# Kernel optimization log

Hardware: AMD Instinct MI355X
Metric: run time of the kernel (lower is better)

Reference implementation:

```python
import jax, jax.numpy as jnp
import numpy as np
import math

B, L, N = 8, 2048, 512
H = 16                                  # router hidden_dim
C = min(16, max(2, int(math.sqrt(N))))  # num_centers = 16
D = 64                                  # d_core
STATIC_TOPK = max(32, int(math.sqrt(N) * 2))  # 45


def setup_inputs() -> dict:
    key = jax.random.key(0)
    ks = jax.random.split(key, 32)
    r = lambda i, shape, s=0.05: jax.random.normal(ks[i], shape, jnp.float32) * s
    return dict(
        x=jax.random.normal(ks[0], (B, L, N), jnp.float32),
        var_embed=r(1, (1, N, H), 0.1),
        temp_w=r(2, (2, H)), temp_b=jnp.zeros((H,), jnp.float32),
        q_w=r(3, (2 * H, H)), q_b=jnp.zeros((H,), jnp.float32),
        k_w=r(4, (2 * H, H)), k_b=jnp.zeros((H,), jnp.float32),
        imp_w=r(5, (2 * H, 1)), imp_b=jnp.zeros((1,), jnp.float32),
        cluster_score=r(6, (N, C), 1.0),
        varproj_w=r(7, (C, D)), varproj_b=jnp.zeros((D,), jnp.float32),
        cp1_w=r(8, (D, D)), cp1_b=jnp.zeros((D,), jnp.float32),
        cp2_w=r(9, (D, D)), cp2_b=jnp.zeros((D,), jnp.float32),
        cg_w=r(10, (N, C * D)), cg_b=jnp.zeros((C * D,), jnp.float32),
        gate_w=r(11, (2 * N, N)), gate_b=jnp.zeros((N,), jnp.float32),
        fus_w=r(12, (N, N)), fus_b=jnp.zeros((N,), jnp.float32),
        ln_g=jnp.ones((N,), jnp.float32), ln_b=jnp.zeros((N,), jnp.float32),
    )


def _build_static_mask(x):
    # torch no_grad block: std over batch dim, unbiased (ddof=1)
    xs = jax.lax.stop_gradient(x)
    x_avg = xs.mean(axis=0)                       # [L, N]
    x_std = jnp.std(xs, axis=0, ddof=1) + 1e-5    # [L, N]
    normed = x_avg / x_std
    sim = normed.T @ normed                       # [N, N]
    sim = sim.at[jnp.diag_indices(N)].set(-1e9)
    _, idx = jax.lax.top_k(sim, STATIC_TOPK)      # [N, STATIC_TOPK]
    return jnp.zeros((N, N), bool).at[jnp.arange(N)[:, None], idx].set(True)


def reference(x, var_embed, temp_w, temp_b, q_w, q_b, k_w, k_b, imp_w, imp_b,
              cluster_score, varproj_w, varproj_b, cp1_w, cp1_b, cp2_w, cp2_b,
              cg_w, cg_b, gate_w, gate_b, fus_w, fus_b, ln_g, ln_b):
    mask = _build_static_mask(x)                  # [N, N] bool

    # ---- SparseVariableRouter ----
    x_var = x.transpose(0, 2, 1)                  # [B, N, L]
    mean = x_var.mean(-1, keepdims=True)
    std = jnp.sqrt(jnp.var(x_var, -1, ddof=1, keepdims=True) + 1e-5)
    time_emb = jnp.concatenate([mean, std], -1) @ temp_w + temp_b   # [B, N, H]
    static_emb = jnp.broadcast_to(var_embed, (x.shape[0], N, H))
    var_fused = jnp.concatenate([static_emb, time_emb], -1)         # [B, N, 2H]
    importance = jax.nn.sigmoid(var_fused @ imp_w + imp_b)[..., 0][:, None, :]  # [B,1,N]
    Q = var_fused @ q_w + q_b
    K = var_fused @ k_w + k_b
    sim = jnp.einsum('bnh,bmh->bnm', Q, K) / math.sqrt(H)
    sim = jnp.where(mask[None], sim, -1e9)
    attn = jax.nn.softmax(sim, axis=-1)
    routed = jnp.einsum('bnm,bml->bnl', attn, x_var).transpose(0, 2, 1)  # [B, L, N]
    ring_out = importance * routed + (1.0 - importance) * x

    # ---- multi-center mixing ----
    summary = x.mean(1)                                        # [B, N]
    center_tokens = (summary @ cg_w + cg_b).reshape(-1, C, D)  # [B, C, D]
    cw = jax.nn.softmax(cluster_score, axis=-1)                # [N, C]
    x_center = jnp.einsum('bln,nc->blc', x, cw) @ varproj_w + varproj_b  # [B, L, D]
    cu = center_tokens[:, None, :, :] + x_center[:, :, None, :]          # [B, L, C, D]
    cu = jax.nn.gelu(cu @ cp1_w + cp1_b, approximate=False) @ cp2_w + cp2_b
    center_to_var = jnp.einsum('blcd,nc->bln', cu, cw)         # [B, L, N]

    # ---- gated fusion + layernorm ----
    gate = jax.nn.sigmoid(jnp.concatenate([ring_out, center_to_var], -1) @ gate_w + gate_b)
    fused = gate * ring_out + (1.0 - gate) * center_to_var
    fused = fused @ fus_w + fus_b
    h = fused + x
    mu = h.mean(-1, keepdims=True)
    var = jnp.var(h, -1, keepdims=True)            # biased, as torch LayerNorm
    out = (h - mu) / jnp.sqrt(var + 1e-5) * ln_g + ln_b
    return out
```

## Files before the change

kernel.cpp:

```cpp
#include <hip/hip_runtime.h>

#define B_ 8
#define L_ 2048
#define N_ 512
#define H_ 16
#define C_ 16
#define D_ 64
#define TK_ 45
#define KS_ 16

typedef __attribute__((ext_vector_type(8))) short bf16x8;
typedef __attribute__((ext_vector_type(4))) float f32x4;

__device__ __forceinline__ float sigmoidf_(float v) { return 1.f / (1.f + expf(-v)); }

__device__ __forceinline__ short f2bf(float f) {
  union { float f; unsigned u; } v; v.f = f;
  unsigned r = (v.u + 0x7fffu + ((v.u >> 16) & 1u)) >> 16;
  return (short)r;
}
__device__ __forceinline__ float bf2f(short s) {
  union { unsigned u; float f; } v; v.u = ((unsigned)(unsigned short)s) << 16;
  return v.f;
}
__device__ __forceinline__ void gload16(const void* g, void* l) {
  __builtin_amdgcn_global_load_lds((const __attribute__((address_space(1))) unsigned int*)g,
                                   (__attribute__((address_space(3))) unsigned int*)l, 16, 0, 0);
}

__global__ __launch_bounds__(512) void k_pre(const float* __restrict__ x,
                                             const float* __restrict__ var_embed,
                                             const float* __restrict__ temp_w,
                                             const float* __restrict__ temp_b,
                                             const float* __restrict__ q_w,
                                             const float* __restrict__ q_b,
                                             const float* __restrict__ k_w,
                                             const float* __restrict__ k_b,
                                             const float* __restrict__ imp_w,
                                             const float* __restrict__ imp_b,
                                             const float* __restrict__ cs,
                                             const float* __restrict__ cp2_w,
                                             const float* __restrict__ cp2_b,
                                             const float* __restrict__ vp_b,
                                             const float* __restrict__ vp_w,
                                             const float* __restrict__ cp1_w,
                                             float* __restrict__ normed,
                                             float* __restrict__ psum,
                                             float* __restrict__ psq,
                                             short* __restrict__ xbf,
                                             float* __restrict__ veq,
                                             float* __restrict__ vek,
                                             float* __restrict__ abc,
                                             float* __restrict__ vei,
                                             float* __restrict__ cw,
                                             float* __restrict__ misc) {
  int blk = blockIdx.x, t = threadIdx.x;
  if (blk < 256) {
    int l0 = blk * 8;
    int n = t;
    float row_s[8] = {}, row_ss[8] = {};
#pragma unroll
    for (int b = 0; b < B_; ++b) {
      float bs = 0.f, bss = 0.f;
#pragma unroll
      for (int r = 0; r < 8; ++r) {
        float v = x[((size_t)b * L_ + l0 + r) * N_ + n];
        bs += v; bss += v * v;
        row_s[r] += v; row_ss[r] += v * v;
        xbf[((size_t)b * L_ + l0 + r) * N_ + n] = f2bf(v);
      }
      psum[((size_t)b * 256 + blk) * N_ + n] = bs;
      psq [((size_t)b * 256 + blk) * N_ + n] = bss;
    }
#pragma unroll
    for (int r = 0; r < 8; ++r) {
      float mean = row_s[r] * (1.f / B_);
      float var  = fmaxf((row_ss[r] - row_s[r] * mean) * (1.f / (B_ - 1)), 0.f);
      normed[(l0 + r) * N_ + n] = mean / (sqrtf(var) + 1e-5f);
    }
    return;
  }
  if (t >= 256) return;
  if (blk < 288) {
    int gid = (blk - 256) * 256 + t;
    int n = gid >> 4, h = gid & 15;
    float aq = 0.f, ak = 0.f;
#pragma unroll
    for (int i = 0; i < 16; ++i) {
      float ve = var_embed[n * 16 + i];
      aq += ve * q_w[i * 16 + h];
      ak += ve * k_w[i * 16 + h];
    }
    veq[gid] = aq;
    vek[gid] = ak;
  } else if (blk == 288) {
    if (t < 16) {
      int h = t;
      float Aq = 0.f, Bq = 0.f, Cq = 0.f, Ak = 0.f, Bk = 0.f, Ck = 0.f;
#pragma unroll
      for (int j = 0; j < 16; ++j) {
        float qw = q_w[(16 + j) * 16 + h];
        float kw = k_w[(16 + j) * 16 + h];
        Aq += temp_w[j] * qw; Bq += temp_w[16 + j] * qw; Cq += temp_b[j] * qw;
        Ak += temp_w[j] * kw; Bk += temp_w[16 + j] * kw; Ck += temp_b[j] * kw;
      }
      abc[h]      = Aq; abc[16 + h] = Bq; abc[32 + h] = Cq + q_b[h];
      abc[48 + h] = Ak; abc[64 + h] = Bk; abc[80 + h] = Ck + k_b[h];
    } else if (t == 16) {
      float aI = 0.f, bI = 0.f, cI = 0.f;
#pragma unroll
      for (int j = 0; j < 16; ++j) {
        float iw = imp_w[16 + j];
        aI += temp_w[j] * iw; bI += temp_w[16 + j] * iw; cI += temp_b[j] * iw;
      }
      abc[96] = aI; abc[97] = bI; abc[98] = cI + imp_b[0];
    }
  } else if (blk < 291) {
    int n = (blk - 289) * 256 + t;
    float a = 0.f;
#pragma unroll
    for (int i = 0; i < 16; ++i)
      a += var_embed[n * 16 + i] * imp_w[i];
    vei[n] = a;
  } else {
#pragma unroll
    for (int u = 0; u < 2; ++u) {
      int n = t + u * 256;
      float v[16], mx = -3e38f;
#pragma unroll
      for (int c = 0; c < 16; ++c) { v[c] = cs[n * 16 + c]; mx = fmaxf(mx, v[c]); }
      float s = 0.f;
#pragma unroll
      for (int c = 0; c < 16; ++c) { v[c] = expf(v[c] - mx); s += v[c]; }
      float inv = 1.f / s;
#pragma unroll
      for (int c = 0; c < 16; ++c) cw[n * 16 + c] = v[c] * inv;
    }
    if (t < 64) {
      float a = 0.f;
#pragma unroll 8
      for (int d = 0; d < 64; ++d) a += cp2_w[t * 64 + d];
      misc[t] = a;
      float vb = 0.f;
#pragma unroll 8
      for (int e = 0; e < 64; ++e) vb += vp_b[e] * cp1_w[e * 64 + t];
      misc[80 + t] = vb;
    }
    if (t == 0) {
      float bsum = 0.f;
      for (int d = 0; d < 64; ++d) bsum += cp2_b[d];
      misc[64] = bsum;
    }
#pragma unroll
    for (int u = 0; u < 4; ++u) {
      int i = t + u * 256;
      int c = i >> 6, d = i & 63;
      float a = 0.f;
#pragma unroll 8
      for (int e = 0; e < 64; ++e) a += vp_w[c * 64 + e] * cp1_w[e * 64 + d];
      misc[96 + i] = a;
    }
  }
}

__global__ __launch_bounds__(256) void k_sim(const float* __restrict__ nrm,
                                             float* __restrict__ simP) {
  __shared__ float As[32 * 64];
  __shared__ float Bs[32 * 64];
  int bx = blockIdx.x;
  int ks = bx >> 6, tile = bx & 63;
  int bi = tile & 7, bj = tile >> 3;
  int t = threadIdx.x, tx = t & 15, ty = t >> 4;
  float acc[4][4] = {};
  int k0 = ks * (L_ / KS_);
  for (int kt = 0; kt < (L_ / KS_) / 32; ++kt) {
    for (int e = t; e < 2048; e += 256) {
      int kk = e >> 6, i = e & 63;
      int krow = k0 + kt * 32 + kk;
      As[e] = nrm[krow * N_ + bi * 64 + i];
      Bs[e] = nrm[krow * N_ + bj * 64 + i];
    }
    __syncthreads();
#pragma unroll
    for (int kk = 0; kk < 32; ++kk) {
      float4 a = *(const float4*)(As + kk * 64 + ty * 4);
      float4 b = *(const float4*)(Bs + kk * 64 + tx * 4);
      float av[4] = {a.x, a.y, a.z, a.w};
      float bv[4] = {b.x, b.y, b.z, b.w};
#pragma unroll
      for (int i = 0; i < 4; ++i)
#pragma unroll
        for (int j = 0; j < 4; ++j)
          acc[i][j] += av[i] * bv[j];
    }
    __syncthreads();
  }
  float* outp = simP + (size_t)ks * (N_ * N_);
#pragma unroll
  for (int i = 0; i < 4; ++i) {
    int row = bi * 64 + ty * 4 + i;
    float4 o = {acc[i][0], acc[i][1], acc[i][2], acc[i][3]};
    *(float4*)(outp + row * N_ + bj * 64 + tx * 4) = o;
  }
}

__global__ __launch_bounds__(256) void k_simred(const float* __restrict__ simP,
                                                float* __restrict__ sim,
                                                const float* __restrict__ psum,
                                                const float* __restrict__ psq,
                                                float* __restrict__ psumR,
                                                float* __restrict__ psqR) {
  int t = threadIdx.x;
  if (blockIdx.x < 256) {
    int gid = blockIdx.x * 256 + t;
    float4 s = {0.f, 0.f, 0.f, 0.f};
#pragma unroll
    for (int ksi = 0; ksi < KS_; ++ksi) {
      float4 p = *(const float4*)(simP + (size_t)ksi * (N_ * N_) + gid * 4);
      s.x += p.x; s.y += p.y; s.z += p.z; s.w += p.w;
    }
    *(float4*)(sim + gid * 4) = s;
    return;
  }
  int tid = (blockIdx.x - 256) * 256 + t;
  const float* src = (tid < 4096) ? psum : psq;
  float* dst = (tid < 4096) ? psumR : psqR;
  int id = tid & 4095;
  int b = id >> 9, n = id & 511;
  float a = 0.f;
#pragma unroll 8
  for (int c = 0; c < 256; ++c)
    a += src[((size_t)b * 256 + c) * N_ + n];
  dst[id] = a;
}

__global__ __launch_bounds__(256) void k_tf(
    const float* __restrict__ sim, int* __restrict__ idx_t,
    const float* __restrict__ psumR, const float* __restrict__ psqR,
    const float* __restrict__ veq, const float* __restrict__ vek,
    const float* __restrict__ abc, const float* __restrict__ vei,
    float* __restrict__ Q, float* __restrict__ Kv,
    float* __restrict__ imp, float* __restrict__ summary) {
  int t = threadIdx.x;
  if (blockIdx.x < 128) {
    int lane = t & 63, wv = t >> 6;
    int n = blockIdx.x * 4 + wv;
    unsigned sv[8];
#pragma unroll
    for (int u = 0; u < 8; ++u) {
      int idx = u * 64 + lane;
      float f = (idx == n) ? -3e38f : sim[n * N_ + idx];
      unsigned xb = __float_as_uint(f);
      sv[u] = (xb & 0x80000000u) ? ~xb : (xb | 0x80000000u);
    }
    unsigned thr = 0u;
#pragma unroll
    for (int b = 31; b >= 0; --b) {
      unsigned cand = thr | (1u << b);
      int cnt = 0;
#pragma unroll
      for (int u = 0; u < 8; ++u)
        cnt += __popcll(__ballot(sv[u] >= cand));
      if (cnt >= TK_) thr = cand;
    }
    int cgt = 0;
#pragma unroll
    for (int u = 0; u < 8; ++u)
      cgt += __popcll(__ballot(sv[u] > thr));
    int need = TK_ - cgt;
    unsigned long long lt_mask = (lane == 0) ? 0ull : (~0ull >> (64 - lane));
    int written = 0, tie_seen = 0;
#pragma unroll
    for (int u = 0; u < 8; ++u) {
      bool gt = sv[u] > thr;
      bool eq = sv[u] == thr;
      unsigned long long me = __ballot(eq);
      bool sel = gt || (eq && (tie_seen + __popcll(me & lt_mask)) < need);
      unsigned long long ms = __ballot(sel);
      int pos = written + __popcll(ms & lt_mask);
      if (sel) idx_t[pos * N_ + n] = u * 64 + lane;
      written += __popcll(ms);
      tie_seen += __popcll(me);
    }
    return;
  }
  int gid = (blockIdx.x - 128) * 256 + t;
  int b = gid >> 9, n = gid & 511;
  float s  = psumR[gid];
  float ss = psqR[gid];
  float mean = s * (1.f / L_);
  float var  = fmaxf((ss - s * mean) * (1.f / (L_ - 1)), 0.f);
  float stdv = sqrtf(var + 1e-5f);
  summary[b * N_ + n] = mean;
#pragma unroll
  for (int h = 0; h < 16; ++h) {
    Q[(b * N_ + n) * 16 + h]  = veq[n * 16 + h] + mean * abc[h]      + stdv * abc[16 + h] + abc[32 + h];
    Kv[(b * N_ + n) * 16 + h] = vek[n * 16 + h] + mean * abc[48 + h] + stdv * abc[64 + h] + abc[80 + h];
  }
  imp[b * N_ + n] = sigmoidf_(vei[n] + mean * abc[96] + stdv * abc[97] + abc[98]);
}

__global__ __launch_bounds__(256) void k_wprep(const float* __restrict__ gate_w,
                                               const float* __restrict__ fus_w,
                                               const float* __restrict__ cw,
                                               const float* __restrict__ misc,
                                               const float* __restrict__ summ,
                                               const float* __restrict__ cg_w,
                                               const float* __restrict__ cg_b,
                                               short* __restrict__ wt_gate,
                                               short* __restrict__ wt_fus,
                                               short* __restrict__ w2t,
                                               short* __restrict__ cwb,
                                               float* __restrict__ ctP) {
  __shared__ float tile[32][33];
  __shared__ float ssum[8][64];
  int blk = blockIdx.x, t = threadIdx.x;
  if (blk < 512) {
    const float* W = (blk < 256) ? gate_w : fus_w;
    short* Wt = (blk < 256) ? wt_gate : wt_fus;
    int ldd = (blk < 256) ? 1024 : 512;
    int b2 = blk & 255;
    int bk = b2 >> 4, bn = b2 & 15;
    int c = t & 31, r = t >> 5;
    for (int rr = r; rr < 32; rr += 8)
      tile[rr][c] = W[(size_t)(bk * 32 + rr) * 512 + bn * 32 + c];
    __syncthreads();
    for (int rr = r; rr < 32; rr += 8)
      Wt[(size_t)(bn * 32 + rr) * ldd + bk * 32 + c] = f2bf(tile[c][rr]);
  } else if (blk < 544) {
    int gid = (blk - 512) * 256 + t;
    int c = gid >> 9, n = gid & 511;
    float a = 0.f;
    for (int m = 0; m < 512; ++m)
      a += cw[m * 16 + c] * gate_w[(size_t)(512 + m) * 512 + n];
    wt_gate[(size_t)n * 1024 + 512 + c] = f2bf(a);
    wt_gate[(size_t)n * 1024 + 528 + c] = 0;
  } else if (blk < 672) {
    int gid = (blk - 544) * 256 + t;
    int d = gid >> 9, m = gid & 511;
    float a = 0.f;
#pragma unroll
    for (int c = 0; c < 16; ++c)
      a += cw[m * 16 + c] * misc[96 + c * 64 + d];
    w2t[d * 512 + m] = f2bf(a);
  } else if (blk < 736) {
    int gid = (blk - 672) * 256 + t;
    int n = gid >> 5, kk = gid & 31;
    cwb[gid] = (kk < 16) ? f2bf(cw[n * 16 + kk]) : (short)0;
  } else {
    int bx = blk - 736;
    int oc = bx & 31;
    int nc = bx >> 5;
    int n0 = nc * 64;
    for (int e = t; e < 512; e += 256)
      ssum[e >> 6][e & 63] = summ[(e >> 6) * 512 + n0 + (e & 63)];
    __syncthreads();
    int b = t >> 5, ol = t & 31;
    int o = oc * 32 + ol;
    float acc = (nc == 0) ? cg_b[o] : 0.f;
#pragma unroll 8
    for (int k = 0; k < 64; ++k)
      acc += ssum[b][k] * cg_w[(size_t)(n0 + k) * 1024 + o];
    ctP[(nc * 8 + b) * 1024 + o] = acc;
  }
}

__global__ __launch_bounds__(256) void k_caxc(const float* __restrict__ ctP,
                                              const float* __restrict__ cp1_w,
                                              const float* __restrict__ cp1_b,
                                              const float* __restrict__ misc,
                                              float* __restrict__ ctp,
                                              const float* __restrict__ Q,
                                              const float* __restrict__ Kv,
                                              const int* __restrict__ idx_t,
                                              short* __restrict__ At,
                                              const short* __restrict__ xbf,
                                              const short* __restrict__ w2t,
                                              float* __restrict__ xcp) {
  __shared__ float cts[256];
  __shared__ short rowbuf[4][512];
  __shared__ __align__(16) short As[2][64 * 32];
  __shared__ __align__(16) short Bs[2][64 * 32];
  int blk = blockIdx.x, t = threadIdx.x;
  if (blk < 32) {
    int row0 = blk * 4;
    int b = row0 >> 4, c0 = row0 & 15;
    {
      int idx = (c0 + (t >> 6)) * 64 + (t & 63);
      float a = 0.f;
#pragma unroll
      for (int p = 0; p < 8; ++p) a += ctP[(p * 8 + b) * 1024 + idx];
      cts[t] = a;
    }
    __syncthreads();
    int lr = t >> 6, d2 = t & 63;
    float a = cp1_b[d2] + misc[80 + d2];
#pragma unroll 8
    for (int d = 0; d < 64; ++d) a += cts[lr * 64 + d] * cp1_w[d * 64 + d2];
    ctp[(row0 + lr) * 64 + d2] = a;
  } else if (blk < 32 + 1024) {
    int w = t >> 6, j = t & 63;
    int bn = (blk - 32) * 4 + w;
    int b = bn >> 9, n = bn & (N_ - 1);
    ((int4*)rowbuf[w])[j] = int4{0, 0, 0, 0};
    float s = -3e38f;
    int m = 0;
    if (j < TK_) {
      m = idx_t[j * N_ + n];
      const float* qp = Q + (b * N_ + n) * H_;
      const float* kp = Kv + (b * N_ + m) * H_;
      float a = 0.f;
#pragma unroll
      for (int h = 0; h < H_; ++h) a += qp[h] * kp[h];
      s = a * 0.25f;
    }
    float mx = s;
#pragma unroll
    for (int o = 32; o > 0; o >>= 1) mx = fmaxf(mx, __shfl_xor(mx, o));
    float e = (j < TK_) ? expf(s - mx) : 0.f;
    float sum = e;
#pragma unroll
    for (int o = 32; o > 0; o >>= 1) sum += __shfl_xor(sum, o);
    __syncthreads();
    if (j < TK_) rowbuf[w][m] = f2bf(e / sum);
    __syncthreads();
    ((int4*)(At + (size_t)bn * 512))[j] = ((int4*)rowbuf[w])[j];
  } else {
    int lane = t & 63, w = t >> 6;
    int lo = lane & 15, hi = lane >> 4;
    int row0 = (blk - 1056) * 64;
    f32x4 acc[4] = {};
    int rA = t >> 2, cA = (t & 3) ^ ((rA >> 1) & 3);
    const short* srcA = xbf + (size_t)(row0 + rA) * 512 + cA * 8;
    const short* srcB = w2t + (size_t)rA * 512 + cA * 8;
    int gl = (lo >> 1) & 3;
    int foff = (lo * 4 + (hi ^ gl)) * 8;
    gload16(srcA, As[0] + t * 8);
    gload16(srcB, Bs[0] + t * 8);
    __syncthreads();
    int cur = 0;
    for (int kt = 0; kt < 16; ++kt) {
      if (kt < 15) {
        gload16(srcA + (kt + 1) * 32, As[cur ^ 1] + t * 8);
        gload16(srcB + (kt + 1) * 32, Bs[cur ^ 1] + t * 8);
      }
      bf16x8 b = *(const bf16x8*)(Bs[cur] + (w * 64) * 8 + foff);
#pragma unroll
      for (int m = 0; m < 4; ++m) {
        bf16x8 a = *(const bf16x8*)(As[cur] + (m * 64) * 8 + foff);
        acc[m] = __builtin_amdgcn_mfma_f32_16x16x32_bf16(a, b, acc[m], 0, 0, 0);
      }
      __syncthreads();
      cur ^= 1;
    }
#pragma unroll
    for (int m = 0; m < 4; ++m)
#pragma unroll
      for (int j = 0; j < 4; ++j) {
        int row = row0 + m * 16 + hi * 4 + j;
        int col = w * 16 + lo;
        xcp[(size_t)row * 64 + col] = acc[m][j];
      }
  }
}

__global__ __launch_bounds__(512) void k_sg(const short* __restrict__ xbf,
                                            const short* __restrict__ At,
                                            const float* __restrict__ imp,
                                            short* __restrict__ abuf,
                                            const float* __restrict__ xcp,
                                            const float* __restrict__ ctp,
                                            const float* __restrict__ misc) {
  __shared__ __align__(16) short As[2][128 * 32];
  __shared__ __align__(16) short Bs[2][128 * 32];
  int blk = blockIdx.x, t = threadIdx.x;
  int lane = t & 63, w = t >> 6;
  if (blk < 512) {
    int lo = lane & 15, hi = lane >> 4;
    int b = blk >> 6;
    int tile = blk & 63;
    int bm = tile >> 2, bn = tile & 3;
    int row0 = b * L_ + bm * 128, n0 = bn * 128;
    int wm = w >> 2, wn = w & 3;
    f32x4 acc[4][2] = {};
    int rs = t >> 2, cs = (t & 3) ^ ((rs >> 1) & 3);
    const short* sA = xbf + (size_t)(row0 + rs) * 512 + cs * 8;
    const short* sB = At + ((size_t)b * N_ + n0 + rs) * 512 + cs * 8;
    int gl = (lo >> 1) & 3;
    int foff = (lo * 4 + (hi ^ gl)) * 8;
    gload16(sA, As[0] + t * 8);
    gload16(sB, Bs[0] + t * 8);
    __syncthreads();
    int cur = 0;
    for (int i = 0; i < 16; ++i) {
      if (i < 15) {
        gload16(sA + (i + 1) * 32, As[cur ^ 1] + t * 8);
        gload16(sB + (i + 1) * 32, Bs[cur ^ 1] + t * 8);
      }
      bf16x8 a[4], bb[2];
#pragma unroll
      for (int m = 0; m < 4; ++m)
        a[m] = *(const bf16x8*)(As[cur] + (wm * 64 + m * 16) * 32 + foff);
#pragma unroll
      for (int n = 0; n < 2; ++n)
        bb[n] = *(const bf16x8*)(Bs[cur] + (wn * 32 + n * 16) * 32 + foff);
#pragma unroll
      for (int m = 0; m < 4; ++m)
#pragma unroll
        for (int n = 0; n < 2; ++n)
          acc[m][n] = __builtin_amdgcn_mfma_f32_16x16x32_bf16(a[m], bb[n], acc[m][n], 0, 0, 0);
      __syncthreads();
      cur ^= 1;
    }
#pragma unroll
    for (int m = 0; m < 4; ++m) {
      int rbase = row0 + wm * 64 + m * 16 + hi * 4;
#pragma unroll
      for (int j = 0; j < 4; ++j) {
        int row = rbase + j;
#pragma unroll
        for (int n = 0; n < 2; ++n) {
          int col = n0 + wn * 32 + n * 16 + lo;
          float iv = imp[b * N_ + col];
          float xv = bf2f(xbf[(size_t)row * 512 + col]);
          abuf[(size_t)row * 1024 + col] = f2bf(iv * acc[m][n][j] + (1.f - iv) * xv);
        }
      }
    }
  } else {
    int row = (blk - 512) * 8 + w;
    int b = row >> 11;
    float v = xcp[(size_t)row * 64 + lane];
    float wgt = misc[lane];
    float bias = misc[64];
    float sval = 0.f;
#pragma unroll
    for (int c = 0; c < 16; ++c) {
      float u = ctp[(b * 16 + c) * 64 + lane] + v;
      float g = 0.5f * u * (1.f + erff(u * 0.70710678118654752f));
      float a = g * wgt;
#pragma unroll
      for (int o = 32; o > 0; o >>= 1) a += __shfl_xor(a, o);
      if (lane == c) sval = a + bias;
    }
    if (lane < 32)
      abuf[(size_t)row * 1024 + 512 + lane] = (lane < 16) ? f2bf(sval) : (short)0;
  }
}

__global__ __launch_bounds__(512) void k_gemm_gate(const short* __restrict__ abuf,
                                                   const short* __restrict__ wt,
                                                   const short* __restrict__ cwb,
                                                   const float* __restrict__ gate_b,
                                                   short* __restrict__ fused_bf) {
  __shared__ __align__(16) short As[2][128 * 32];
  __shared__ __align__(16) short Bs[2][128 * 32];
  int t = threadIdx.x, lane = t & 63, w = t >> 6;
  int lo = lane & 15, hi = lane >> 4;
  int bm = blockIdx.x >> 2, bn = blockIdx.x & 3;
  int row0 = bm * 128, n0 = bn * 128;
  int wm = w >> 2, wn = w & 3;
  f32x4 acc[4][2] = {};
  f32x4 acc2[4][2] = {};
  int rs = t >> 2, cs = (t & 3) ^ ((rs >> 1) & 3);
  const short* sA = abuf + (size_t)(row0 + rs) * 1024 + cs * 8;
  const short* sB = wt + (size_t)(n0 + rs) * 1024 + cs * 8;
  int gl = (lo >> 1) & 3;
  int foff = (lo * 4 + (hi ^ gl)) * 8;
  gload16(sA + 16 * 32, As[0] + t * 8);
  gload16(cwb + (size_t)(n0 + rs) * 32 + cs * 8, Bs[0] + t * 8);
  gload16(sA, As[1] + t * 8);
  gload16(sB, Bs[1] + t * 8);
  __syncthreads();
  {
    bf16x8 a[4], bb[2];
#pragma unroll
    for (int m = 0; m < 4; ++m)
      a[m] = *(const bf16x8*)(As[0] + (wm * 64 + m * 16) * 32 + foff);
#pragma unroll
    for (int n = 0; n < 2; ++n)
      bb[n] = *(const bf16x8*)(Bs[0] + (wn * 32 + n * 16) * 32 + foff);
#pragma unroll
    for (int m = 0; m < 4; ++m)
#pragma unroll
      for (int n = 0; n < 2; ++n)
        acc2[m][n] = __builtin_amdgcn_mfma_f32_16x16x32_bf16(a[m], bb[n], acc2[m][n], 0, 0, 0);
  }
  __syncthreads();
  int cur = 1;
  for (int i = 1; i <= 17; ++i) {
    if (i < 17) {
      gload16(sA + i * 32, As[cur ^ 1] + t * 8);
      gload16(sB + i * 32, Bs[cur ^ 1] + t * 8);
    }
    bf16x8 a[4], bb[2];
#pragma unroll
    for (int m = 0; m < 4; ++m)
      a[m] = *(const bf16x8*)(As[cur] + (wm * 64 + m * 16) * 32 + foff);
#pragma unroll
    for (int n = 0; n < 2; ++n)
      bb[n] = *(const bf16x8*)(Bs[cur] + (wn * 32 + n * 16) * 32 + foff);
#pragma unroll
    for (int m = 0; m < 4; ++m)
#pragma unroll
      for (int n = 0; n < 2; ++n)
        acc[m][n] = __builtin_amdgcn_mfma_f32_16x16x32_bf16(a[m], bb[n], acc[m][n], 0, 0, 0);
    __syncthreads();
    cur ^= 1;
  }
#pragma unroll
  for (int m = 0; m < 4; ++m) {
    int rbase = row0 + wm * 64 + m * 16 + hi * 4;
#pragma unroll
    for (int j = 0; j < 4; ++j) {
      int row = rbase + j;
#pragma unroll
      for (int n = 0; n < 2; ++n) {
        int col = n0 + wn * 32 + n * 16 + lo;
        float g = sigmoidf_(acc[m][n][j] + gate_b[col]);
        float ringv = bf2f(abuf[(size_t)row * 1024 + col]);
        fused_bf[(size_t)row * 512 + col] = f2bf(g * ringv + (1.f - g) * acc2[m][n][j]);
      }
    }
  }
}

__global__ __launch_bounds__(512) void k_gemm_fus(const short* __restrict__ fused_bf,
                                                  const short* __restrict__ wtf,
                                                  const float* __restrict__ x,
                                                  const float* __restrict__ fus_b,
                                                  const float* __restrict__ ln_g,
                                                  const float* __restrict__ ln_b,
                                                  float* __restrict__ out) {
  __shared__ __align__(16) short As[2][64 * 32];
  __shared__ __align__(16) short Bs[2][512 * 32];
  __shared__ float Ssh[8][64], Qsh[8][64];
  __shared__ float mus[64], rss[64];
  int t = threadIdx.x, lane = t & 63, w = t >> 6;
  int lo = lane & 15, hi = lane >> 4;
  int row0 = blockIdx.x * 64;
  f32x4 acc[4][4] = {};
  int pA = w * 64 + lane;
  int rA = pA >> 2, cA = (pA & 3) ^ ((rA >> 1) & 3);
  const short* srcA = fused_bf + (size_t)(row0 + rA) * 512 + cA * 8;
  int rB[4], cB[4];
  const short* srcB[4];
#pragma unroll
  for (int q = 0; q < 4; ++q) {
    int pB = w * 256 + q * 64 + lane;
    rB[q] = pB >> 2; cB[q] = (pB & 3) ^ ((rB[q] >> 1) & 3);
    srcB[q] = wtf + (size_t)rB[q] * 512 + cB[q] * 8;
  }
  int gl = (lo >> 1) & 3;
  int foff = (lo * 4 + (hi ^ gl)) * 8;
  if (w < 4) gload16(srcA, As[0] + pA * 8);
#pragma unroll
  for (int q = 0; q < 4; ++q)
    gload16(srcB[q], Bs[0] + (w * 256 + q * 64) * 8);
  __syncthreads();
  int cur = 0;
  for (int i = 0; i < 16; ++i) {
    if (i < 15) {
      int kt = i + 1;
      if (w < 4) gload16(srcA + kt * 32, As[cur ^ 1] + pA * 8);
#pragma unroll
      for (int q = 0; q < 4; ++q)
        gload16(srcB[q] + kt * 32, Bs[cur ^ 1] + (w * 256 + q * 64) * 8);
    }
    bf16x8 a[4], b[4];
#pragma unroll
    for (int m = 0; m < 4; ++m)
      a[m] = *(const bf16x8*)(As[cur] + (m * 64) * 8 + foff);
#pragma unroll
    for (int n = 0; n < 4; ++n)
      b[n] = *(const bf16x8*)(Bs[cur] + (w * 256 + n * 64) * 8 + foff);
#pragma unroll
    for (int m = 0; m < 4; ++m)
#pragma unroll
      for (int n = 0; n < 4; ++n)
        acc[m][n] = __builtin_amdgcn_mfma_f32_16x16x32_bf16(a[m], b[n], acc[m][n], 0, 0, 0);
    __syncthreads();
    cur ^= 1;
  }
#pragma unroll
  for (int m = 0; m < 4; ++m) {
#pragma unroll
    for (int j = 0; j < 4; ++j) {
      int rl = m * 16 + hi * 4 + j;
      int row = row0 + rl;
      float ps = 0.f, pq = 0.f;
#pragma unroll
      for (int n = 0; n < 4; ++n) {
        int col = w * 64 + n * 16 + lo;
        float h = acc[m][n][j] + fus_b[col] + x[(size_t)row * 512 + col];
        acc[m][n][j] = h;
        ps += h; pq += h * h;
      }
#pragma unroll
      for (int o = 1; o < 16; o <<= 1) {
        ps += __shfl_xor(ps, o);
        pq += __shfl_xor(pq, o);
      }
      if (lo == 0) { Ssh[w][rl] = ps; Qsh[w][rl] = pq; }
    }
  }
  __syncthreads();
  if (t < 64) {
    float s = 0.f, q = 0.f;
#pragma unroll
    for (int ww = 0; ww < 8; ++ww) { s += Ssh[ww][t]; q += Qsh[ww][t]; }
    float mu = s * (1.f / N_);
    float var = q * (1.f / N_) - mu * mu;
    mus[t] = mu;
    rss[t] = rsqrtf(fmaxf(var, 0.f) + 1e-5f);
  }
  __syncthreads();
#pragma unroll
  for (int m = 0; m < 4; ++m) {
#pragma unroll
    for (int j = 0; j < 4; ++j) {
      int rl = m * 16 + hi * 4 + j;
      int row = row0 + rl;
      float mu = mus[rl], rs = rss[rl];
#pragma unroll
      for (int n = 0; n < 4; ++n) {
        int col = w * 64 + n * 16 + lo;
        out[(size_t)row * 512 + col] = (acc[m][n][j] - mu) * rs * ln_g[col] + ln_b[col];
      }
    }
  }
}

extern "C" void kernel_launch(void* const* d_in, const int* in_sizes, int n_in,
                              void* d_out, int out_size, void* d_ws, size_t ws_size,
                              hipStream_t stream) {
  (void)in_sizes; (void)n_in; (void)out_size; (void)ws_size;
  const float* x         = (const float*)d_in[0];
  const float* var_embed = (const float*)d_in[1];
  const float* temp_w    = (const float*)d_in[2];
  const float* temp_b    = (const float*)d_in[3];
  const float* q_w       = (const float*)d_in[4];
  const float* q_b       = (const float*)d_in[5];
  const float* k_w       = (const float*)d_in[6];
  const float* k_b       = (const float*)d_in[7];
  const float* imp_w     = (const float*)d_in[8];
  const float* imp_b     = (const float*)d_in[9];
  const float* cluster   = (const float*)d_in[10];
  const float* vp_w      = (const float*)d_in[11];
  const float* vp_b      = (const float*)d_in[12];
  const float* cp1_w     = (const float*)d_in[13];
  const float* cp1_b     = (const float*)d_in[14];
  const float* cp2_w     = (const float*)d_in[15];
  const float* cp2_b     = (const float*)d_in[16];
  const float* cg_w      = (const float*)d_in[17];
  const float* cg_b      = (const float*)d_in[18];
  const float* gate_w    = (const float*)d_in[19];
  const float* gate_b    = (const float*)d_in[20];
  const float* fus_w     = (const float*)d_in[21];
  const float* fus_b     = (const float*)d_in[22];
  const float* ln_g      = (const float*)d_in[23];
  const float* ln_b      = (const float*)d_in[24];
  float* out = (float*)d_out;
  float* ws  = (float*)d_ws;

  float* normed = ws + 0;
  int*   idx_t  = (int*)(ws + 1310720);
  float* Qb     = ws + 1335296;
  float* Kb     = ws + 1400832;
  float* impb   = ws + 1466368;
  float* summ   = ws + 1470464;
  float* cw     = ws + 1658880;
  float* ctp    = ws + 1675264;
  float* misc   = ws + 1683456;
  short* w2t    = (short*)(ws + 1693696);
  short* cwb    = (short*)(ws + 1710080);
  short* abuf     = (short*)(ws + 1720320);
  short* fused_bf = (short*)(ws + 10108928);
  short* wt_gate  = (short*)(ws + 14303232);
  short* wt_fus   = (short*)(ws + 14565376);
  float* ctP      = ws + 15220736;
  short* At       = (short*)(ws + 15286272);
  float* sim      = ws + 16334848;
  float* veq      = ws + 16596992;
  float* vek      = ws + 16605184;
  float* abc      = ws + 16613376;
  float* vei      = ws + 16613504;
  float* psum     = ws + 17000000;
  float* psq      = ws + 18100000;
  float* psumR    = ws + 19200000;
  float* psqR     = ws + 19210000;
  float* simP = (float*)abuf;
  float* xcp  = normed;
  short* xbf  = fused_bf;

  k_pre<<<292, 512, 0, stream>>>(x, var_embed, temp_w, temp_b, q_w, q_b, k_w, k_b,
                                 imp_w, imp_b, cluster, cp2_w, cp2_b, vp_b, vp_w,
                                 cp1_w, normed, psum, psq, xbf, veq, vek, abc, vei,
                                 cw, misc);
  k_sim<<<64 * KS_, 256, 0, stream>>>(normed, simP);
  k_simred<<<288, 256, 0, stream>>>(simP, sim, psum, psq, psumR, psqR);
  k_tf<<<144, 256, 0, stream>>>(sim, idx_t, psumR, psqR, veq, vek, abc, vei,
                                Qb, Kb, impb, summ);
  k_wprep<<<992, 256, 0, stream>>>(gate_w, fus_w, cw, misc, summ, cg_w, cg_b,
                                   wt_gate, wt_fus, w2t, cwb, ctP);
  k_caxc<<<1312, 256, 0, stream>>>(ctP, cp1_w, cp1_b, misc, ctp, Qb, Kb, idx_t,
                                   At, xbf, w2t, xcp);
  k_sg<<<2560, 512, 0, stream>>>(xbf, At, impb, abuf, xcp, ctp, misc);
  k_gemm_gate<<<512, 512, 0, stream>>>(abuf, wt_gate, cwb, gate_b, fused_bf);
  k_gemm_fus<<<256, 512, 0, stream>>>(fused_bf, wt_fus, x, fus_b, ln_g, ln_b, out);
}
```

Baseline: 195.1 us.

## Split k_pre finer, remap GEMM blocks across XCDs, restructure center-path tail

k_pre now gives 4 rows per block instead of 8, so it launches twice as many blocks to raise parallelism. The partial-sum buffers double in size, and the reduction loop in k_simred gets twice as long. The GEMM kernels remap block IDs so that consecutive blocks are spread across the 8 XCDs, aiming for better L2 locality. The center-path tail of k_sg now stages xcp and ctp tiles in shared memory and has each thread compute one (row, center) output, replacing the per-wave shuffle reductions and cutting the grid from 2560 to 1024 blocks.

```diff
diff --git a/kernel.cpp b/kernel.cpp
--- a/kernel.cpp
+++ b/kernel.cpp
@@ -55,25 +55,25 @@
                                              float* __restrict__ cw,
                                              float* __restrict__ misc) {
   int blk = blockIdx.x, t = threadIdx.x;
-  if (blk < 256) {
-    int l0 = blk * 8;
+  if (blk < 512) {
+    int l0 = blk * 4;
     int n = t;
-    float row_s[8] = {}, row_ss[8] = {};
+    float row_s[4] = {}, row_ss[4] = {};
 #pragma unroll
     for (int b = 0; b < B_; ++b) {
       float bs = 0.f, bss = 0.f;
 #pragma unroll
-      for (int r = 0; r < 8; ++r) {
+      for (int r = 0; r < 4; ++r) {
         float v = x[((size_t)b * L_ + l0 + r) * N_ + n];
         bs += v; bss += v * v;
         row_s[r] += v; row_ss[r] += v * v;
         xbf[((size_t)b * L_ + l0 + r) * N_ + n] = f2bf(v);
       }
-      psum[((size_t)b * 256 + blk) * N_ + n] = bs;
-      psq [((size_t)b * 256 + blk) * N_ + n] = bss;
-    }
-#pragma unroll
-    for (int r = 0; r < 8; ++r) {
+      psum[((size_t)b * 512 + blk) * N_ + n] = bs;
+      psq [((size_t)b * 512 + blk) * N_ + n] = bss;
+    }
+#pragma unroll
+    for (int r = 0; r < 4; ++r) {
       float mean = row_s[r] * (1.f / B_);
       float var  = fmaxf((row_ss[r] - row_s[r] * mean) * (1.f / (B_ - 1)), 0.f);
       normed[(l0 + r) * N_ + n] = mean / (sqrtf(var) + 1e-5f);
@@ -81,8 +81,8 @@
     return;
   }
   if (t >= 256) return;
-  if (blk < 288) {
-    int gid = (blk - 256) * 256 + t;
+  if (blk < 544) {
+    int gid = (blk - 512) * 256 + t;
     int n = gid >> 4, h = gid & 15;
     float aq = 0.f, ak = 0.f;
 #pragma unroll
@@ -93,7 +93,7 @@
     }
     veq[gid] = aq;
     vek[gid] = ak;
-  } else if (blk == 288) {
+  } else if (blk == 544) {
     if (t < 16) {
       int h = t;
       float Aq = 0.f, Bq = 0.f, Cq = 0.f, Ak = 0.f, Bk = 0.f, Ck = 0.f;
@@ -115,8 +115,8 @@
       }
       abc[96] = aI; abc[97] = bI; abc[98] = cI + imp_b[0];
     }
-  } else if (blk < 291) {
-    int n = (blk - 289) * 256 + t;
+  } else if (blk < 547) {
+    int n = (blk - 545) * 256 + t;
     float a = 0.f;
 #pragma unroll
     for (int i = 0; i < 16; ++i)
@@ -229,8 +229,8 @@
   int b = id >> 9, n = id & 511;
   float a = 0.f;
 #pragma unroll 8
-  for (int c = 0; c < 256; ++c)
-    a += src[((size_t)b * 256 + c) * N_ + n];
+  for (int c = 0; c < 512; ++c)
+    a += src[((size_t)b * 512 + c) * N_ + n];
   dst[id] = a;
 }
 
@@ -476,9 +476,10 @@
   int blk = blockIdx.x, t = threadIdx.x;
   int lane = t & 63, w = t >> 6;
   if (blk < 512) {
+    int vid = ((blk & 7) << 6) | (blk >> 3);
     int lo = lane & 15, hi = lane >> 4;
-    int b = blk >> 6;
-    int tile = blk & 63;
+    int b = vid >> 6;
+    int tile = vid & 63;
     int bm = tile >> 2, bn = tile & 3;
     int row0 = b * L_ + bm * 128, n0 = bn * 128;
     int wm = w >> 2, wn = w & 3;
@@ -528,23 +529,30 @@
       }
     }
   } else {
-    int row = (blk - 512) * 8 + w;
-    int b = row >> 11;
-    float v = xcp[(size_t)row * 64 + lane];
-    float wgt = misc[lane];
-    float bias = misc[64];
-    float sval = 0.f;
-#pragma unroll
-    for (int c = 0; c < 16; ++c) {
-      float u = ctp[(b * 16 + c) * 64 + lane] + v;
+    float* xcps = (float*)As;
+    float* ctps = (float*)Bs;
+    float* cp2sd = ((float*)Bs) + 1100;
+    int row0 = (blk - 512) * 32;
+    int b = row0 >> 11;
+    for (int e = t; e < 32 * 64; e += 512)
+      xcps[(e >> 6) * 65 + (e & 63)] = xcp[(size_t)(row0 + (e >> 6)) * 64 + (e & 63)];
+    for (int e = t; e < 16 * 64; e += 512)
+      ctps[(e >> 6) * 65 + (e & 63)] = ctp[b * 1024 + e];
+    if (t < 65) cp2sd[t] = misc[t];
+    __syncthreads();
+    int r = t >> 4, c = t & 15;
+    const float* xr = xcps + r * 65;
+    const float* cc = ctps + c * 65;
+    float acc = 0.f;
+#pragma unroll 8
+    for (int d = 0; d < 64; ++d) {
+      float u = cc[d] + xr[d];
       float g = 0.5f * u * (1.f + erff(u * 0.70710678118654752f));
-      float a = g * wgt;
-#pragma unroll
-      for (int o = 32; o > 0; o >>= 1) a += __shfl_xor(a, o);
-      if (lane == c) sval = a + bias;
-    }
-    if (lane < 32)
-      abuf[(size_t)row * 1024 + 512 + lane] = (lane < 16) ? f2bf(sval) : (short)0;
+      acc += g * cp2sd[d];
+    }
+    int row = row0 + r;
+    abuf[(size_t)row * 1024 + 512 + c] = f2bf(acc + cp2sd[64]);
+    abuf[(size_t)row * 1024 + 528 + c] = 0;
   }
 }
 
@@ -557,7 +565,8 @@
   __shared__ __align__(16) short Bs[2][128 * 32];
   int t = threadIdx.x, lane = t & 63, w = t >> 6;
   int lo = lane & 15, hi = lane >> 4;
-  int bm = blockIdx.x >> 2, bn = blockIdx.x & 3;
+  int vid = ((blockIdx.x & 7) << 6) | (blockIdx.x >> 3);
+  int bm = vid >> 2, bn = vid & 3;
   int row0 = bm * 128, n0 = bn * 128;
   int wm = w >> 2, wn = w & 3;
   f32x4 acc[4][2] = {};
@@ -638,7 +647,8 @@
   __shared__ float mus[64], rss[64];
   int t = threadIdx.x, lane = t & 63, w = t >> 6;
   int lo = lane & 15, hi = lane >> 4;
-  int row0 = blockIdx.x * 64;
+  int vid = ((blockIdx.x & 7) << 5) | (blockIdx.x >> 3);
+  int row0 = vid * 64;
   f32x4 acc[4][4] = {};
   int pA = w * 64 + lane;
   int rA = pA >> 2, cA = (pA & 3) ^ ((rA >> 1) & 3);
@@ -786,14 +796,14 @@
   float* abc      = ws + 16613376;
   float* vei      = ws + 16613504;
   float* psum     = ws + 17000000;
-  float* psq      = ws + 18100000;
-  float* psumR    = ws + 19200000;
-  float* psqR     = ws + 19210000;
+  float* psq      = ws + 19200000;
+  float* psumR    = ws + 21400000;
+  float* psqR     = ws + 21410000;
   float* simP = (float*)abuf;
   float* xcp  = normed;
   short* xbf  = fused_bf;
 
-  k_pre<<<292, 512, 0, stream>>>(x, var_embed, temp_w, temp_b, q_w, q_b, k_w, k_b,
+  k_pre<<<548, 512, 0, stream>>>(x, var_embed, temp_w, temp_b, q_w, q_b, k_w, k_b,
                                  imp_w, imp_b, cluster, cp2_w, cp2_b, vp_b, vp_w,
                                  cp1_w, normed, psum, psq, xbf, veq, vek, abc, vei,
                                  cw, misc);
@@ -805,7 +815,7 @@
                                    wt_gate, wt_fus, w2t, cwb, ctP);
   k_caxc<<<1312, 256, 0, stream>>>(ctP, cp1_w, cp1_b, misc, ctp, Qb, Kb, idx_t,
                                    At, xbf, w2t, xcp);
-  k_sg<<<2560, 512, 0, stream>>>(xbf, At, impb, abuf, xcp, ctp, misc);
+  k_sg<<<1024, 512, 0, stream>>>(xbf, At, impb, abuf, xcp, ctp, misc);
   k_gemm_gate<<<512, 512, 0, stream>>>(abuf, wt_gate, cwb, gate_b, fused_bf);
   k_gemm_fus<<<256, 512, 0, stream>>>(fused_bf, wt_fus, x, fus_b, ln_g, ln_b, out);
 }
```

New measurement: 190.4 us. 1.02x faster.
